# Kernel optimization log

Measured on AMD Instinct MI355X. Metric: run time of the kernel, lower is better.

Reference implementation:

```python
import jax, jax.numpy as jnp
import numpy as np

HIDDEN = 2048
HEADS = 16
HEAD_DIM = HIDDEN // HEADS
TOP_K = 256
B, N = 1, 2048


def setup_inputs() -> dict:
    key = jax.random.key(0)
    ks = jax.random.split(key, 9)
    s = 0.02
    return {
        "hidden_states": jax.random.normal(ks[0], (B, N, HIDDEN), jnp.float32),
        "Wq": jax.random.normal(ks[1], (HIDDEN, HIDDEN), jnp.float32) * s,
        "bq": jnp.zeros((HIDDEN,), jnp.float32),
        "Wk": jax.random.normal(ks[2], (HIDDEN, HIDDEN), jnp.float32) * s,
        "bk": jnp.zeros((HIDDEN,), jnp.float32),
        "Wv": jax.random.normal(ks[3], (HIDDEN, HIDDEN), jnp.float32) * s,
        "bv": jnp.zeros((HIDDEN,), jnp.float32),
        "Wo": jax.random.normal(ks[4], (HIDDEN, HIDDEN), jnp.float32) * s,
        "bo": jnp.zeros((HIDDEN,), jnp.float32),
    }


def _split_heads(x):
    b, n, _ = x.shape
    return x.reshape(b, n, HEADS, HEAD_DIM).transpose(0, 2, 1, 3)  # b h n d


def reference(hidden_states, Wq, bq, Wk, bk, Wv, bv, Wo, bo):
    scale = 1.0 / jnp.sqrt(jnp.float32(HEAD_DIM))
    q = _split_heads(hidden_states @ Wq + bq)  # [b,h,n,d]
    k = _split_heads(hidden_states @ Wk + bk)
    v = _split_heads(hidden_states @ Wv + bv)

    # Sparse path (kv_seq_length > attention_window): dense QK^T used only to rank keys.
    scores = jnp.einsum("bhnd,bhmd->bhnm", q, k) * scale  # [b,h,n,n]
    importance = scores.mean(axis=2)  # [b,h,n] aggregate over queries
    _, idx = jax.lax.top_k(importance, TOP_K)  # [b,h,k]

    # gather selected K/V (torch.gather along seq dim)
    k_sel = jnp.take_along_axis(k, idx[..., None], axis=2)  # [b,h,k,d]
    v_sel = jnp.take_along_axis(v, idx[..., None], axis=2)

    w = jax.nn.softmax(jnp.einsum("bhnd,bhkd->bhnk", q, k_sel) * scale, axis=-1)
    out = jnp.einsum("bhnk,bhkd->bhnd", w, v_sel)  # [b,h,n,d]
    out = out.transpose(0, 2, 1, 3).reshape(hidden_states.shape[0], -1, HIDDEN)
    return out @ Wo + bo
```

## Files before the change

### kernel.cpp

```cpp
#include <hip/hip_runtime.h>


typedef __attribute__((ext_vector_type(8))) short bf16x8;
typedef __attribute__((ext_vector_type(4))) float f32x4;

__device__ __forceinline__ unsigned short f2bf(float x) {
    unsigned u = __float_as_uint(x);
    u += 0x7fffu + ((u >> 16) & 1u);
    return (unsigned short)(u >> 16);
}

__device__ __forceinline__ void load_lds16(const unsigned short* g, unsigned short* l) {
    __builtin_amdgcn_global_load_lds(
        (const __attribute__((address_space(1))) unsigned int*)g,
        (__attribute__((address_space(3))) unsigned int*)l,
        16, 0, 0);
}

struct Ptr4  { const float* p[4]; };

__global__ __launch_bounds__(256) void gemm_qkv(
    const unsigned short* __restrict__ HSb,
    const unsigned short* __restrict__ WT4,
    const float* __restrict__ bq,
    const float* __restrict__ bk,
    const float* __restrict__ bv,
    const int* __restrict__ idx,
    unsigned short* __restrict__ Qb,
    unsigned short* __restrict__ Ksel,
    unsigned short* __restrict__ VselT)
{
    __shared__ __align__(16) unsigned short As[2][128][32];
    __shared__ __align__(16) unsigned short Bs[2][128][32];

    const int tid  = threadIdx.x;
    const int lane = tid & 63;
    const int wave = tid >> 6;
    const int wm = wave >> 1, wn = wave & 1;
    const int lr = lane >> 2;
    const int lc = (lane & 3) * 8;

    const int bid = blockIdx.x;

    int kv, h = 0, bm, bn;
    const unsigned short* Bt;
    long ar0, ar1;
    if (bid < 64) {
        kv = 1 + (bid >> 5);
        const int t = bid & 31;
        h  = t >> 1;
        bm = (t & 1) * 128;
        bn = h * 128;
        Bt = WT4 + (long)kv * 4194304;
        ar0 = idx[h * 256 + bm + wave * 16 + lr];
        ar1 = idx[h * 256 + bm + wave * 16 + 64 + lr];
    } else {
        kv = 0;
        const int t = bid - 64;
        const int st = t >> 4, u = t & 15;
        bm = ((st >> 2) * 4 + (u >> 2)) * 128;
        bn = ((st & 3) * 4 + (u & 3)) * 128;
        Bt = WT4;
        ar0 = bm + wave * 16 + lr;
        ar1 = ar0 + 64;
    }

    const unsigned short* Arow0 = HSb + ar0 * 2048 + lc;
    const unsigned short* Arow1 = HSb + ar1 * 2048 + lc;
    const unsigned short* Brow0 = Bt + (long)(bn + wave * 16 + lr) * 2048 + lc;
    const unsigned short* Brow1 = Brow0 + 64 * 2048;

    f32x4 acc[4][4];
#pragma unroll
    for (int i = 0; i < 4; i++)
#pragma unroll
        for (int j = 0; j < 4; j++) acc[i][j] = f32x4{0.f, 0.f, 0.f, 0.f};

    auto stage = [&](int b, int k0) {
        load_lds16(Arow0 + k0, &As[b][wave * 16][0]);
        load_lds16(Brow0 + k0, &Bs[b][wave * 16][0]);
        load_lds16(Arow1 + k0, &As[b][wave * 16 + 64][0]);
        load_lds16(Brow1 + k0, &Bs[b][wave * 16 + 64][0]);
    };
    auto compute = [&](int b) {
        bf16x8 af[4], bf[4];
#pragma unroll
        for (int s = 0; s < 4; s++)
            af[s] = *(const bf16x8*)&As[b][wm * 64 + s * 16 + (lane & 15)][(lane >> 4) * 8];
#pragma unroll
        for (int t = 0; t < 4; t++)
            bf[t] = *(const bf16x8*)&Bs[b][wn * 64 + t * 16 + (lane & 15)][(lane >> 4) * 8];
#pragma unroll
        for (int s = 0; s < 4; s++)
#pragma unroll
            for (int t = 0; t < 4; t++)
                acc[s][t] = __builtin_amdgcn_mfma_f32_16x16x32_bf16(af[s], bf[t], acc[s][t], 0, 0, 0);
    };

    stage(0, 0);
    for (int t = 0; t < 64; t += 2) {
        __syncthreads();
        stage(1, (t + 1) * 32);
        asm volatile("" ::: "memory");
        compute(0);
        __syncthreads();
        if (t + 2 < 64) stage(0, (t + 2) * 32);
        asm volatile("" ::: "memory");
        compute(1);
    }

    if (kv == 0) {
#pragma unroll
        for (int s = 0; s < 4; s++) {
#pragma unroll
            for (int t = 0; t < 4; t++) {
                const int col  = bn + wn * 64 + t * 16 + (lane & 15);
                const int row0 = bm + wm * 64 + s * 16 + (lane >> 4) * 4;
                const float bb = bq[col];
#pragma unroll
                for (int r = 0; r < 4; r++)
                    Qb[(long)(row0 + r) * 2048 + col] = f2bf(acc[s][t][r] + bb);
            }
        }
    } else {
        const float* bp = (kv == 1) ? bk : bv;
#pragma unroll
        for (int s = 0; s < 4; s++) {
#pragma unroll
            for (int t = 0; t < 4; t++) {
                const int col = bn + wn * 64 + t * 16 + (lane & 15);
                const int dd  = col & 127;
                const float bb = bp[col];
                const int j0 = bm + wm * 64 + s * 16 + (lane >> 4) * 4;
#pragma unroll
                for (int r = 0; r < 4; r++) {
                    const int j = j0 + r;
                    const unsigned short h16 = f2bf(acc[s][t][r] + bb);
                    if (kv == 1) Ksel [h * 32768 + j * 128 + dd] = h16;
                    else         VselT[h * 32768 + dd * 256 + j] = h16;
                }
            }
        }
    }
}

__global__ __launch_bounds__(256) void gemm_o(
    const unsigned short* __restrict__ Att,
    const unsigned short* __restrict__ WoT,
    float* __restrict__ Opart)
{
    __shared__ __align__(16) unsigned short As[2][128][32];
    __shared__ __align__(16) unsigned short Bs[2][128][32];

    const int tid  = threadIdx.x;
    const int lane = tid & 63;
    const int wave = tid >> 6;
    const int wm = wave >> 1, wn = wave & 1;
    const int lr = lane >> 2;
    const int lc = (lane & 3) * 8;

    const int bm = blockIdx.y * 128;
    const int bn = blockIdx.x * 128;
    const int b  = blockIdx.z;

    const unsigned short* Arow0 = Att + b * 1024 + (long)(bm + wave * 16 + lr) * 2048 + lc;
    const unsigned short* Arow1 = Arow0 + 64 * 2048;
    const unsigned short* Brow0 = WoT + b * 1024 + (long)(bn + wave * 16 + lr) * 2048 + lc;
    const unsigned short* Brow1 = Brow0 + 64 * 2048;

    f32x4 acc[4][4];
#pragma unroll
    for (int i = 0; i < 4; i++)
#pragma unroll
        for (int j = 0; j < 4; j++) acc[i][j] = f32x4{0.f, 0.f, 0.f, 0.f};

    auto stage = [&](int bb, int k0) {
        load_lds16(Arow0 + k0, &As[bb][wave * 16][0]);
        load_lds16(Brow0 + k0, &Bs[bb][wave * 16][0]);
        load_lds16(Arow1 + k0, &As[bb][wave * 16 + 64][0]);
        load_lds16(Brow1 + k0, &Bs[bb][wave * 16 + 64][0]);
    };
    auto compute = [&](int bb) {
        bf16x8 af[4], bf[4];
#pragma unroll
        for (int s = 0; s < 4; s++)
            af[s] = *(const bf16x8*)&As[bb][wm * 64 + s * 16 + (lane & 15)][(lane >> 4) * 8];
#pragma unroll
        for (int t = 0; t < 4; t++)
            bf[t] = *(const bf16x8*)&Bs[bb][wn * 64 + t * 16 + (lane & 15)][(lane >> 4) * 8];
#pragma unroll
        for (int s = 0; s < 4; s++)
#pragma unroll
            for (int t = 0; t < 4; t++)
                acc[s][t] = __builtin_amdgcn_mfma_f32_16x16x32_bf16(af[s], bf[t], acc[s][t], 0, 0, 0);
    };

    stage(0, 0);
    for (int t = 0; t < 32; t += 2) {
        __syncthreads();
        stage(1, (t + 1) * 32);
        asm volatile("" ::: "memory");
        compute(0);
        __syncthreads();
        if (t + 2 < 32) stage(0, (t + 2) * 32);
        asm volatile("" ::: "memory");
        compute(1);
    }

#pragma unroll
    for (int s = 0; s < 4; s++) {
#pragma unroll
        for (int t = 0; t < 4; t++) {
            const int col  = bn + wn * 64 + t * 16 + (lane & 15);
            const int row0 = bm + wm * 64 + s * 16 + (lane >> 4) * 4;
#pragma unroll
            for (int r = 0; r < 4; r++)
                Opart[(long)b * 4194304 + (long)(row0 + r) * 2048 + col] = acc[s][t][r];
        }
    }
}

__global__ __launch_bounds__(256) void oreduce(const float* __restrict__ part,
                                               const float* __restrict__ bo,
                                               float* __restrict__ out) {
    const long i = ((long)blockIdx.x * 256 + threadIdx.x) * 4;
    float4 a = *(const float4*)(part + i);
    float4 b = *(const float4*)(part + 4194304 + i);
    const int col = (int)(i & 2047);
    float4 o;
    o.x = a.x + b.x + bo[col];
    o.y = a.y + b.y + bo[col + 1];
    o.z = a.z + b.z + bo[col + 2];
    o.w = a.w + b.w + bo[col + 3];
    *(float4*)(out + i) = o;
}

#define QS_OFF(c)  ((c) * 2048)
#define KS_OFF(c)  (4096 + (c) * 8192)
#define PS_OFF     0
#define VS_OFF(c)  (16896 + (c) * 4096)

__global__ __launch_bounds__(256, 2) void attn_kernel(
    const unsigned short* __restrict__ Qb,
    const unsigned short* __restrict__ Ksel,
    const unsigned short* __restrict__ VselT,
    unsigned short* __restrict__ Att)
{
    __shared__ __align__(16) unsigned short smem[25088];
    __shared__ float linv[64];

    const int tid  = threadIdx.x;
    const int lane = tid & 63;
    const int wave = tid >> 6;
    const int bm = blockIdx.x * 64;
    const int h  = blockIdx.y;
    const int lr = lane >> 2, lc = (lane & 3) * 8;

    const unsigned short* Kh = Ksel  + h * 32768;
    const unsigned short* Vh = VselT + h * 32768;

    f32x4 acc[16];
#pragma unroll
    for (int t = 0; t < 16; t++) acc[t] = f32x4{0.f, 0.f, 0.f, 0.f};

#pragma unroll
    for (int c2 = 0; c2 < 2; c2++) {
        __syncthreads();
#pragma unroll
        for (int c = 0; c < 2; c++) {
            const int k0 = c2 * 64 + c * 32;
            load_lds16(Qb + (long)(bm + wave * 16 + lr) * 2048 + h * 128 + k0 + lc,
                       &smem[QS_OFF(c) + wave * 512]);
#pragma unroll
            for (int q = 0; q < 4; q++)
                load_lds16(Kh + (wave * 64 + q * 16 + lr) * 128 + k0 + lc,
                           &smem[KS_OFF(c) + (wave * 64 + q * 16) * 32]);
        }
        __syncthreads();
#pragma unroll
        for (int kk = 0; kk < 2; kk++) {
            bf16x8 af = *(const bf16x8*)&smem[QS_OFF(kk) + (wave * 16 + (lane & 15)) * 32 + (lane >> 4) * 8];
#pragma unroll
            for (int t = 0; t < 16; t++) {
                bf16x8 bfv = *(const bf16x8*)&smem[KS_OFF(kk) + (t * 16 + (lane & 15)) * 32 + (lane >> 4) * 8];
                acc[t] = __builtin_amdgcn_mfma_f32_16x16x32_bf16(af, bfv, acc[t], 0, 0, 0);
            }
        }
    }
    __syncthreads();

    const float se = 0.08838834764831845f * 1.4426950408889634f;
#pragma unroll
    for (int r = 0; r < 4; r++) {
        float mx = -3.0e38f;
#pragma unroll
        for (int t = 0; t < 16; t++) mx = fmaxf(mx, acc[t][r]);
#pragma unroll
        for (int off = 1; off < 16; off <<= 1) mx = fmaxf(mx, __shfl_xor(mx, off));
        float sum = 0.f;
#pragma unroll
        for (int t = 0; t < 16; t++) {
            float p = exp2f((acc[t][r] - mx) * se);
            acc[t][r] = p;
            sum += p;
        }
#pragma unroll
        for (int off = 1; off < 16; off <<= 1) sum += __shfl_xor(sum, off);
        const int row = wave * 16 + (lane >> 4) * 4 + r;
#pragma unroll
        for (int t = 0; t < 16; t++)
            smem[PS_OFF + row * 264 + t * 16 + (lane & 15)] = f2bf(acc[t][r]);
        if ((lane & 15) == 0) linv[row] = 1.0f / sum;
    }

    const int wm2 = wave >> 1, wn2 = wave & 1;
    f32x4 acc2[2][4];
#pragma unroll
    for (int i = 0; i < 2; i++)
#pragma unroll
        for (int j = 0; j < 4; j++) acc2[i][j] = f32x4{0.f, 0.f, 0.f, 0.f};

#pragma unroll
    for (int c2 = 0; c2 < 4; c2++) {
#pragma unroll
        for (int c = 0; c < 2; c++) {
            const int j0 = c2 * 64 + c * 32;
#pragma unroll
            for (int q = 0; q < 2; q++)
                load_lds16(Vh + (wave * 32 + q * 16 + lr) * 256 + j0 + lc,
                           &smem[VS_OFF(c) + (wave * 32 + q * 16) * 32]);
        }
        __syncthreads();
#pragma unroll
        for (int c = 0; c < 2; c++) {
            const int j0 = c2 * 64 + c * 32;
            bf16x8 af2[2], bf2v[4];
#pragma unroll
            for (int s2 = 0; s2 < 2; s2++)
                af2[s2] = *(const bf16x8*)&smem[PS_OFF + (wm2 * 32 + s2 * 16 + (lane & 15)) * 264 + j0 + (lane >> 4) * 8];
#pragma unroll
            for (int t2 = 0; t2 < 4; t2++)
                bf2v[t2] = *(const bf16x8*)&smem[VS_OFF(c) + (wn2 * 64 + t2 * 16 + (lane & 15)) * 32 + (lane >> 4) * 8];
#pragma unroll
            for (int s2 = 0; s2 < 2; s2++)
#pragma unroll
                for (int t2 = 0; t2 < 4; t2++)
                    acc2[s2][t2] = __builtin_amdgcn_mfma_f32_16x16x32_bf16(af2[s2], bf2v[t2], acc2[s2][t2], 0, 0, 0);
        }
        __syncthreads();
    }

#pragma unroll
    for (int s2 = 0; s2 < 2; s2++) {
#pragma unroll
        for (int t2 = 0; t2 < 4; t2++) {
            const int d = wn2 * 64 + t2 * 16 + (lane & 15);
#pragma unroll
            for (int r = 0; r < 4; r++) {
                const int row = wm2 * 32 + s2 * 16 + (lane >> 4) * 4 + r;
                float v = acc2[s2][t2][r] * linv[row];
                Att[(long)(bm + row) * 2048 + h * 128 + d] = f2bf(v);
            }
        }
    }
}

__global__ __launch_bounds__(256) void prep_kernel(Ptr4 srcs, unsigned short* __restrict__ WT4,
                                                   const float* __restrict__ hs,
                                                   double* __restrict__ part) {
    const int b = blockIdx.x;
    const int tid = threadIdx.x;
    if (b < 4096) {
        __shared__ float tile[64][65];
        const int z = b >> 10, xy = b & 1023;
        const float* W = srcs.p[z];
        unsigned short* WT = WT4 + (long)z * 4194304;
        const int bx = (xy & 31) * 64;
        const int by = (xy >> 5) * 64;
        const int x = tid & 63, y = tid >> 6;
#pragma unroll
        for (int i = 0; i < 64; i += 4)
            tile[y + i][x] = W[(long)(by + y + i) * 2048 + bx + x];
        __syncthreads();
#pragma unroll
        for (int i = 0; i < 64; i += 4)
            WT[(long)(bx + y + i) * 2048 + by + x] = f2bf(tile[x][y + i]);
    } else {
        const int c = b - 4096;
        const int col = (c & 7) * 256 + tid;
        const int r0  = (c >> 3) * 32;
        double a = 0.0;
#pragma unroll 4
        for (int r = 0; r < 32; r++) a += (double)hs[(long)(r0 + r) * 2048 + col];
        part[(long)(c >> 3) * 2048 + col] = a;
    }
}

__global__ void fill_kernel(float* p, float v, long n) {
    long i = ((long)blockIdx.x * blockDim.x + threadIdx.x) * 4;
    if (i + 3 < n) { p[i] = v; p[i+1] = v; p[i+2] = v; p[i+3] = v; }
}

__global__ __launch_bounds__(256) void mean_qsum_part(const double* __restrict__ part,
                                                      const float* __restrict__ Wq,
                                                      double* __restrict__ partq) {
    __shared__ float hsb[32];
    const int j  = blockIdx.x * 256 + threadIdx.x;
    const int i0 = blockIdx.y * 32;
    if (threadIdx.x < 32) {
        double s = 0.0;
#pragma unroll 4
        for (int g = 0; g < 64; g++) s += part[(long)g * 2048 + i0 + threadIdx.x];
        hsb[threadIdx.x] = (float)(s * (1.0 / 2048.0));
    }
    __syncthreads();
    double a = 0.0;
#pragma unroll 4
    for (int r = 0; r < 32; r++)
        a += (double)hsb[r] * (double)Wq[(long)(i0 + r) * 2048 + j];
    partq[(long)blockIdx.y * 2048 + j] = a;
}

__global__ void qsum_fin(const double* __restrict__ partq, const float* __restrict__ bq,
                         float* __restrict__ qbar) {
    const int j = blockIdx.x * 64 + threadIdx.x;
    double s = (double)bq[j];
#pragma unroll 4
    for (int g = 0; g < 64; g++) s += partq[(long)g * 2048 + j];
    qbar[j] = (float)s;
}

__global__ __launch_bounds__(256) void u_kernel(const float* __restrict__ Wk,
                                                const float* __restrict__ qbar,
                                                float* __restrict__ U) {
    const int i = blockIdx.x, t = threadIdx.x;
#pragma unroll
    for (int r = 0; r < 2; r++) {
        const int e = r * 1024 + t * 4;
        float4 w = *(const float4*)(Wk + (long)i * 2048 + e);
        float4 q = *(const float4*)(qbar + e);
        float a = w.x * q.x + w.y * q.y + w.z * q.z + w.w * q.w;
#pragma unroll
        for (int off = 16; off; off >>= 1) a += __shfl_xor(a, off);
        if ((t & 31) == 0) U[(long)i * 16 + r * 8 + (t >> 5)] = a;
    }
}

__global__ __launch_bounds__(256) void cast_imp_kernel(const float* __restrict__ hs,
                                                       const float* __restrict__ U,
                                                       unsigned short* __restrict__ HSb,
                                                       float* __restrict__ imp) {
    __shared__ float row[2048];
    __shared__ float red[4][16];
    const int m = blockIdx.x, t = threadIdx.x;
    for (int i = t; i < 2048; i += 256) {
        float v = hs[(long)m * 2048 + i];
        row[i] = v;
        HSb[(long)m * 2048 + i] = f2bf(v);
    }
    __syncthreads();
    float p[16];
#pragma unroll
    for (int h = 0; h < 16; h++) p[h] = 0.f;
    for (int i = t * 8; i < t * 8 + 8; i++) {
        const float v = row[i];
        const float* u = U + i * 16;
#pragma unroll
        for (int h = 0; h < 16; h++) p[h] += v * u[h];
    }
#pragma unroll
    for (int off = 32; off; off >>= 1)
#pragma unroll
        for (int h = 0; h < 16; h++) p[h] += __shfl_down(p[h], off);
    if ((t & 63) == 0)
#pragma unroll
        for (int h = 0; h < 16; h++) red[t >> 6][h] = p[h];
    __syncthreads();
    if (t < 16)
        imp[(long)t * 2048 + m] = red[0][t] + red[1][t] + red[2][t] + red[3][t];
}

__global__ __launch_bounds__(64) void topk_idx(const float* __restrict__ imp,
                                               int* __restrict__ idx) {
    const int h = blockIdx.x;
    const int lane = threadIdx.x;
    unsigned u[32];
#pragma unroll
    for (int r = 0; r < 32; r++) {
        unsigned x = __float_as_uint(imp[(long)h * 2048 + r * 64 + lane]);
        u[r] = (x & 0x80000000u) ? ~x : (x | 0x80000000u);
    }
    unsigned cur = 0;
    for (int b = 31; b >= 0; b--) {
        const unsigned cand = cur | (1u << b);
        int tot = 0;
#pragma unroll
        for (int r = 0; r < 32; r++)
            tot += (int)__popcll(__ballot(u[r] >= cand));
        if (tot >= 256) cur = cand;
    }
    const unsigned long long below = (1ull << lane) - 1ull;
    int pos[32];
    int base = 0;
#pragma unroll
    for (int r = 0; r < 32; r++) {
        const bool q = u[r] > cur;
        const unsigned long long m = __ballot(q);
        pos[r] = q ? base + (int)__popcll(m & below) : -1;
        base += (int)__popcll(m);
    }
#pragma unroll
    for (int r = 0; r < 32; r++) {
        const bool q = (u[r] == cur);
        const unsigned long long m = __ballot(q);
        if (q) {
            const int p = base + (int)__popcll(m & below);
            pos[r] = (p < 256) ? p : -1;
        }
        base += (int)__popcll(m);
    }
#pragma unroll
    for (int r = 0; r < 32; r++)
        if (pos[r] >= 0) idx[h * 256 + pos[r]] = r * 64 + lane;
}

extern "C" void kernel_launch(void* const* d_in, const int* in_sizes, int n_in,
                              void* d_out, int out_size, void* d_ws, size_t ws_size,
                              hipStream_t stream)
{
    const float* hs = (const float*)d_in[0];
    const float* Wq = (const float*)d_in[1];
    const float* bq = (const float*)d_in[2];
    const float* Wk = (const float*)d_in[3];
    const float* bk = (const float*)d_in[4];
    const float* Wv = (const float*)d_in[5];
    const float* bv = (const float*)d_in[6];
    const float* Wo = (const float*)d_in[7];
    const float* bo = (const float*)d_in[8];

    char* ws = (char*)d_ws;
    size_t off = 0;
    auto alloc = [&](size_t b) -> void* {
        void* p = ws + off;
        off = (off + b + 255) & ~(size_t)255;
        return p;
    };
    unsigned short* HSb   = (unsigned short*)alloc(8388608);
    unsigned short* WT4   = (unsigned short*)alloc(4 * 8388608);
    unsigned short* Qb    = (unsigned short*)alloc(8388608);
    unsigned short* Att   = (unsigned short*)alloc(8388608);
    unsigned short* Ksel  = (unsigned short*)alloc(1048576);
    unsigned short* VselT = (unsigned short*)alloc(1048576);
    float* Opart = (float*)alloc(2 * 16777216);
    double* part  = (double*)alloc(1048576);
    double* partq = (double*)alloc(1048576);
    float* qbar  = (float*)alloc(8192);
    float* U     = (float*)alloc(131072);
    float* imp   = (float*)alloc(131072);
    int*   idx   = (int*)alloc(16384);

    if (off > ws_size) {
        fill_kernel<<<4096, 256, 0, stream>>>((float*)d_out, 12345.0f, (long)out_size);
        return;
    }

    unsigned short* WoT = WT4 + 3 * 4194304;

    prep_kernel<<<4608, 256, 0, stream>>>(Ptr4{{Wq, Wk, Wv, Wo}}, WT4, hs, part);

    mean_qsum_part<<<dim3(8, 64), 256, 0, stream>>>(part, Wq, partq);
    qsum_fin<<<32, 64, 0, stream>>>(partq, bq, qbar);
    u_kernel<<<2048, 256, 0, stream>>>(Wk, qbar, U);
    cast_imp_kernel<<<2048, 256, 0, stream>>>(hs, U, HSb, imp);

    topk_idx<<<16, 64, 0, stream>>>(imp, idx);

    gemm_qkv<<<320, 256, 0, stream>>>(HSb, WT4, bq, bk, bv, idx, Qb, Ksel, VselT);

    attn_kernel<<<dim3(32, 16), 256, 0, stream>>>(Qb, Ksel, VselT, Att);

    gemm_o<<<dim3(16, 16, 2), 256, 0, stream>>>(Att, WoT, Opart);

    oreduce<<<4096, 256, 0, stream>>>(Opart, bo, (float*)d_out);
}
```

Measured before the change: 323.3 us.

## Deepen GEMM LDS pipeline to four stages with explicit vmcnt waits

Both the QKV and output-projection GEMMs move from a double-buffered LDS scheme to a four-buffer ring. Three k-steps are prefetched ahead, and each step waits with an explicit s_waitcnt vmcnt before a raw s_barrier. The loop is guarded by sched_barriers and ends with a drain epilogue for the last three steps. The aim is to hide more global-load latency behind MFMA work, at the cost of doubling shared memory per block to 64KB, which may lower occupancy.

```diff
diff --git a/kernel.cpp b/kernel.cpp
--- a/kernel.cpp
+++ b/kernel.cpp
@@ -30,8 +30,8 @@
     unsigned short* __restrict__ Ksel,
     unsigned short* __restrict__ VselT)
 {
-    __shared__ __align__(16) unsigned short As[2][128][32];
-    __shared__ __align__(16) unsigned short Bs[2][128][32];
+    __shared__ __align__(16) unsigned short As[4][128][32];
+    __shared__ __align__(16) unsigned short Bs[4][128][32];
 
     const int tid  = threadIdx.x;
     const int lane = tid & 63;
@@ -76,7 +76,8 @@
 #pragma unroll
         for (int j = 0; j < 4; j++) acc[i][j] = f32x4{0.f, 0.f, 0.f, 0.f};
 
-    auto stage = [&](int b, int k0) {
+    auto stage = [&](int b, int step) {
+        const int k0 = step * 32;
         load_lds16(Arow0 + k0, &As[b][wave * 16][0]);
         load_lds16(Brow0 + k0, &Bs[b][wave * 16][0]);
         load_lds16(Arow1 + k0, &As[b][wave * 16 + 64][0]);
@@ -98,16 +99,29 @@
     };
 
     stage(0, 0);
-    for (int t = 0; t < 64; t += 2) {
-        __syncthreads();
-        stage(1, (t + 1) * 32);
-        asm volatile("" ::: "memory");
-        compute(0);
-        __syncthreads();
-        if (t + 2 < 64) stage(0, (t + 2) * 32);
-        asm volatile("" ::: "memory");
-        compute(1);
-    }
+    stage(1, 1);
+    stage(2, 2);
+#pragma unroll 4
+    for (int t = 0; t < 61; ++t) {
+        asm volatile("s_waitcnt vmcnt(8)" ::: "memory");
+        __builtin_amdgcn_s_barrier();
+        __builtin_amdgcn_sched_barrier(0);
+        stage((t + 3) & 3, t + 3);
+        __builtin_amdgcn_sched_barrier(0);
+        compute(t & 3);
+    }
+    asm volatile("s_waitcnt vmcnt(8)" ::: "memory");
+    __builtin_amdgcn_s_barrier();
+    __builtin_amdgcn_sched_barrier(0);
+    compute(1);
+    asm volatile("s_waitcnt vmcnt(4)" ::: "memory");
+    __builtin_amdgcn_s_barrier();
+    __builtin_amdgcn_sched_barrier(0);
+    compute(2);
+    asm volatile("s_waitcnt vmcnt(0)" ::: "memory");
+    __builtin_amdgcn_s_barrier();
+    __builtin_amdgcn_sched_barrier(0);
+    compute(3);
 
     if (kv == 0) {
 #pragma unroll
@@ -149,8 +163,8 @@
     const unsigned short* __restrict__ WoT,
     float* __restrict__ Opart)
 {
-    __shared__ __align__(16) unsigned short As[2][128][32];
-    __shared__ __align__(16) unsigned short Bs[2][128][32];
+    __shared__ __align__(16) unsigned short As[4][128][32];
+    __shared__ __align__(16) unsigned short Bs[4][128][32];
 
     const int tid  = threadIdx.x;
     const int lane = tid & 63;
@@ -174,7 +188,8 @@
 #pragma unroll
         for (int j = 0; j < 4; j++) acc[i][j] = f32x4{0.f, 0.f, 0.f, 0.f};
 
-    auto stage = [&](int bb, int k0) {
+    auto stage = [&](int bb, int step) {
+        const int k0 = step * 32;
         load_lds16(Arow0 + k0, &As[bb][wave * 16][0]);
         load_lds16(Brow0 + k0, &Bs[bb][wave * 16][0]);
         load_lds16(Arow1 + k0, &As[bb][wave * 16 + 64][0]);
@@ -196,16 +211,29 @@
     };
 
     stage(0, 0);
-    for (int t = 0; t < 32; t += 2) {
-        __syncthreads();
-        stage(1, (t + 1) * 32);
-        asm volatile("" ::: "memory");
-        compute(0);
-        __syncthreads();
-        if (t + 2 < 32) stage(0, (t + 2) * 32);
-        asm volatile("" ::: "memory");
-        compute(1);
-    }
+    stage(1, 1);
+    stage(2, 2);
+#pragma unroll 4
+    for (int t = 0; t < 29; ++t) {
+        asm volatile("s_waitcnt vmcnt(8)" ::: "memory");
+        __builtin_amdgcn_s_barrier();
+        __builtin_amdgcn_sched_barrier(0);
+        stage((t + 3) & 3, t + 3);
+        __builtin_amdgcn_sched_barrier(0);
+        compute(t & 3);
+    }
+    asm volatile("s_waitcnt vmcnt(8)" ::: "memory");
+    __builtin_amdgcn_s_barrier();
+    __builtin_amdgcn_sched_barrier(0);
+    compute(1);
+    asm volatile("s_waitcnt vmcnt(4)" ::: "memory");
+    __builtin_amdgcn_s_barrier();
+    __builtin_amdgcn_sched_barrier(0);
+    compute(2);
+    asm volatile("s_waitcnt vmcnt(0)" ::: "memory");
+    __builtin_amdgcn_s_barrier();
+    __builtin_amdgcn_sched_barrier(0);
+    compute(3);
 
 #pragma unroll
     for (int s = 0; s < 4; s++) {
```

Measured after the change: 310.7 us. -3.9%, faster.
